# Performance work log

Hardware: AMD Instinct MI355X
Metric: run time of the kernel (lower is better)

The kernel has to match this reference:

```python
import jax, jax.numpy as jnp
import numpy as np

B = 16384
R, N_NODES, K, N_LAYERS, LATENT = 5, 68, 32, 3, 68


def setup_inputs() -> dict:
    key = jax.random.key(0)
    ks = jax.random.split(key, 6)
    z = jax.random.normal(ks[0], (B, LATENT), dtype=jnp.float32)
    adjacency = jax.random.randint(ks[1], (N_NODES, K), 0, N_NODES)
    # init_fc weights stored as [latent, n_nodes] so forward is z @ fc_w[r] + fc_b[r]
    fc_w = jax.random.normal(ks[2], (R, LATENT, N_NODES), dtype=jnp.float32) * 0.1
    fc_b = jax.random.normal(ks[3], (R, N_NODES), dtype=jnp.float32) * 0.1
    gcn_w = jax.random.normal(ks[4], (R, N_LAYERS, N_NODES, K), dtype=jnp.float32) * 0.1
    gcn_b = jax.random.normal(ks[5], (R, N_LAYERS, N_NODES), dtype=jnp.float32) * 0.1
    return {"z": z, "adjacency": adjacency, "fc_w": fc_w, "fc_b": fc_b,
            "gcn_w": gcn_w, "gcn_b": gcn_b}


def _gcn_layer(x, adjacency, w, b):
    # x: [B, N]; adjacency: [N, K] int; w: [N, K]; b: [N]
    x_nb = x[:, adjacency]                      # [B, N, K] ragged-style gather
    val = jnp.einsum('bnk,nk->bn', x_nb, w) + b  # per-node weighted neighbor sum
    return jax.nn.sigmoid(val)


def reference(z, adjacency, fc_w, fc_b, gcn_w, gcn_b):
    b = z.shape[0]
    sc_sum = jnp.zeros((b, N_NODES, N_NODES), dtype=z.dtype)
    for r in range(R):
        x = z @ fc_w[r] + fc_b[r]               # init_fc[r]
        for l in range(N_LAYERS):
            x = _gcn_layer(x, adjacency, gcn_w[r, l], gcn_b[r, l])
        # rank-1 outer product per sample: bmm(x.unsqueeze(2), x.unsqueeze(1))
        sc_sum = sc_sum + x[:, :, None] * x[:, None, :]
    sc_sum = 0.5 * (sc_sum + jnp.swapaxes(sc_sum, 1, 2))
    return sc_sum.reshape(b, -1)
```

## Files before the change

kernel.cpp:

```cpp
#include <hip/hip_runtime.h>
#include <math.h>

#define R_ 5
#define NN 68
#define KK 32
#define NL 3
#define LAT 68
#define NSL 17
#define ROWQ (NN / 4)
#define NF4 ((NN * NN) / 4)
#define BBK2 16
#define LSTR 344
#define NPREP (R_ * NL)

__global__ __launch_bounds__(256) void prep_k(
    const float* __restrict__ z, const int* __restrict__ adj,
    const float* __restrict__ gw, float* __restrict__ wd,
    float* __restrict__ zT, int B) {
  const int t = threadIdx.x;
  if (blockIdx.x < NPREP) {
    const int rl = blockIdx.x;
    __shared__ float col[NN][NN + 4];
    for (int i = t; i < NN * (NN + 4); i += 256) (&col[0][0])[i] = 0.0f;
    __syncthreads();
    if (t < NN) {
      const int n = t;
      const int* ar = adj + n * KK;
      const float* wr = gw + ((size_t)rl * NN + n) * KK;
      for (int k = 0; k < KK; ++k) col[ar[k]][n] += wr[k];
    }
    __syncthreads();
    float* wout = wd + (size_t)rl * NN * NN;
    for (int i = t; i < NN * NN; i += 256) {
      const int m = i / NN, n = i - m * NN;
      wout[i] = col[m][n];
    }
  } else {
    const int b0 = (blockIdx.x - NPREP) * 64;
    __shared__ float zls[64][LAT + 1];
    for (int idx = t; idx < 64 * ROWQ; idx += 256) {
      const int row = idx / ROWQ, q = idx - row * ROWQ;
      const float4 v =
          *reinterpret_cast<const float4*>(z + (size_t)(b0 + row) * LAT + 4 * q);
      zls[row][4 * q + 0] = v.x;
      zls[row][4 * q + 1] = v.y;
      zls[row][4 * q + 2] = v.z;
      zls[row][4 * q + 3] = v.w;
    }
    __syncthreads();
    for (int idx = t; idx < LAT * 64; idx += 256) {
      const int l = idx >> 6, bb = idx & 63;
      zT[(size_t)l * B + b0 + bb] = zls[bb][l];
    }
  }
}

__global__ __launch_bounds__(256) void chain_k(
    const float* __restrict__ zT, const float* __restrict__ fc_w,
    const float* __restrict__ fc_b, const float* __restrict__ wd,
    const float* __restrict__ gb, float* __restrict__ X, int B, int nb) {
  const int t = threadIdx.x;
  const int lane = t & 63;
  const int w = __builtin_amdgcn_readfirstlane(t >> 6);
  const int n0 = w * NSL;
  const int r = blockIdx.x / nb;
  const int b0 = (blockIdx.x - r * nb) * 64;

  __shared__ float xs[NN][64];

  for (int idx = t; idx < NN * 64; idx += 256) {
    const int m = idx >> 6;
    xs[m][idx & 63] = zT[(size_t)m * B + b0 + (idx & 63)];
  }
  __syncthreads();

  float acc[NSL];

#pragma unroll 1
  for (int stage = 0; stage < 1 + NL; ++stage) {
    const float* wb = (stage == 0) ? fc_w + (size_t)r * LAT * NN
                                   : wd + (size_t)(r * NL + stage - 1) * NN * NN;
    const float* bias = (stage == 0) ? fc_b + r * NN
                                     : gb + (size_t)(r * NL + stage - 1) * NN;
#pragma unroll
    for (int j = 0; j < NSL; ++j) acc[j] = bias[n0 + j];

#pragma unroll 1
    for (int mb = 0; mb < 4; ++mb) {
      float xmv[NSL];
#pragma unroll
      for (int k = 0; k < NSL; ++k) xmv[k] = xs[mb * NSL + k][lane];
      const float* wrb = wb + (size_t)(mb * NSL) * NN + n0;
#pragma unroll
      for (int k = 0; k < NSL; ++k) {
        const float* wr = wrb + (size_t)k * NN;
#pragma unroll
        for (int j = 0; j < NSL; ++j) acc[j] = fmaf(xmv[k], wr[j], acc[j]);
      }
    }
    if (stage > 0) {
#pragma unroll
      for (int j = 0; j < NSL; ++j)
        acc[j] = 1.0f / (1.0f + __expf(-acc[j]));
    }
    if (stage < NL) {
      __syncthreads();
#pragma unroll
      for (int j = 0; j < NSL; ++j) xs[n0 + j][lane] = acc[j];
      __syncthreads();
    }
  }

  float* Xb = X + ((size_t)r * NN + n0) * B + b0 + lane;
#pragma unroll
  for (int j = 0; j < NSL; ++j) Xb[(size_t)j * B] = acc[j];
}

__global__ __launch_bounds__(256) void outer_k(const float* __restrict__ X,
                                               float* __restrict__ out, int B) {
  const int t = threadIdx.x;
  const int b0 = blockIdx.x * BBK2;
  __shared__ float xls[BBK2 * LSTR];

  for (int idx = t; idx < R_ * NN * BBK2; idx += 256) {
    const int rn = idx >> 4, bb = idx & (BBK2 - 1);
    xls[bb * LSTR + rn] = X[(size_t)rn * B + b0 + bb];
  }
  __syncthreads();

  float4* ob = reinterpret_cast<float4*>(out) + (size_t)b0 * NF4;
  const int total = BBK2 * NF4;
  for (int fg = t; fg < total; fg += 256) {
    const int bb = fg / NF4;
    const int f = fg - bb * NF4;
    const int i = f / ROWQ;
    const int q = f - i * ROWQ;
    const float* xb = &xls[bb * LSTR];
    float4 a = make_float4(0.f, 0.f, 0.f, 0.f);
#pragma unroll
    for (int r = 0; r < R_; ++r) {
      const float xi = xb[r * NN + i];
      const float4 xj = *reinterpret_cast<const float4*>(xb + r * NN + 4 * q);
      a.x = fmaf(xi, xj.x, a.x);
      a.y = fmaf(xi, xj.y, a.y);
      a.z = fmaf(xi, xj.z, a.z);
      a.w = fmaf(xi, xj.w, a.w);
    }
    ob[fg] = a;
  }
}

extern "C" void kernel_launch(void* const* d_in, const int* in_sizes, int n_in,
                              void* d_out, int out_size, void* d_ws, size_t ws_size,
                              hipStream_t stream) {
  const float* z    = (const float*)d_in[0];
  const int*   adj  = (const int*)  d_in[1];
  const float* fc_w = (const float*)d_in[2];
  const float* fc_b = (const float*)d_in[3];
  const float* gw   = (const float*)d_in[4];
  const float* gb   = (const float*)d_in[5];
  float* out = (float*)d_out;

  const int B = in_sizes[0] / LAT;
  float* wd = (float*)d_ws;
  float* zT = wd + R_ * NL * NN * NN;
  float* X  = zT + (size_t)LAT * B;

  const int nb = B / 64;

  prep_k<<<NPREP + B / 64, 256, 0, stream>>>(z, adj, gw, wd, zT, B);
  chain_k<<<R_ * nb, 256, 0, stream>>>(zT, fc_w, fc_b, wd, gb, X, B, nb);
  outer_k<<<B / BBK2, 256, 0, stream>>>(X, out, B);
}
```

Measured before the change: 126.6 us.

## Restructure outer-product kernel to compute 4-row tiles with register-held columns

The outer_k kernel now assigns each wave 4 samples, with each lane holding its column slice of x in registers across all 17 row groups. Each row group is computed as a 4-row tile and staged in a per-wave LDS buffer, then written to global memory as contiguous float4 stores. This cuts the per-element index divisions and repeated LDS loads of the original flat loop. In exchange it adds divergent work for the 16-column tail (done only by c==0 lanes) and extra LDS round trips for the staged output.

```diff
diff --git a/kernel.cpp b/kernel.cpp
--- a/kernel.cpp
+++ b/kernel.cpp
@@ -121,6 +121,7 @@
   const int t = threadIdx.x;
   const int b0 = blockIdx.x * BBK2;
   __shared__ float xls[BBK2 * LSTR];
+  __shared__ float obuf[4][4 * 272];
 
   for (int idx = t; idx < R_ * NN * BBK2; idx += 256) {
     const int rn = idx >> 4, bb = idx & (BBK2 - 1);
@@ -128,25 +129,65 @@
   }
   __syncthreads();
 
-  float4* ob = reinterpret_cast<float4*>(out) + (size_t)b0 * NF4;
-  const int total = BBK2 * NF4;
-  for (int fg = t; fg < total; fg += 256) {
-    const int bb = fg / NF4;
-    const int f = fg - bb * NF4;
-    const int i = f / ROWQ;
-    const int q = f - i * ROWQ;
-    const float* xb = &xls[bb * LSTR];
-    float4 a = make_float4(0.f, 0.f, 0.f, 0.f);
-#pragma unroll
-    for (int r = 0; r < R_; ++r) {
-      const float xi = xb[r * NN + i];
-      const float4 xj = *reinterpret_cast<const float4*>(xb + r * NN + 4 * q);
-      a.x = fmaf(xi, xj.x, a.x);
-      a.y = fmaf(xi, xj.y, a.y);
-      a.z = fmaf(xi, xj.z, a.z);
-      a.w = fmaf(xi, xj.w, a.w);
-    }
-    ob[fg] = a;
+  const int lane = t & 63;
+  const int wv = t >> 6;
+  const int bsub = lane >> 4;
+  const int bb = wv * 4 + bsub;
+  const int c = lane & 15;
+  const float* xb = &xls[bb * LSTR];
+
+  float4 xj[R_], xj16[R_];
+#pragma unroll
+  for (int r = 0; r < R_; ++r)
+    xj[r] = *reinterpret_cast<const float4*>(xb + r * NN + 4 * c);
+#pragma unroll
+  for (int r = 0; r < R_; ++r)
+    xj16[r] = *reinterpret_cast<const float4*>(xb + r * NN + 64);
+
+  float* ow = &obuf[wv][0];
+  const float4* ow4 = reinterpret_cast<const float4*>(ow);
+  float4* out4 = reinterpret_cast<float4*>(out);
+
+#pragma unroll 1
+  for (int g = 0; g < 17; ++g) {
+    float4 xi[R_];
+#pragma unroll
+    for (int r = 0; r < R_; ++r)
+      xi[r] = *reinterpret_cast<const float4*>(xb + r * NN + 4 * g);
+#pragma unroll
+    for (int k = 0; k < 4; ++k) {
+      float4 a = make_float4(0.f, 0.f, 0.f, 0.f);
+#pragma unroll
+      for (int r = 0; r < R_; ++r) {
+        const float s = reinterpret_cast<const float*>(&xi[r])[k];
+        a.x = fmaf(s, xj[r].x, a.x);
+        a.y = fmaf(s, xj[r].y, a.y);
+        a.z = fmaf(s, xj[r].z, a.z);
+        a.w = fmaf(s, xj[r].w, a.w);
+      }
+      *reinterpret_cast<float4*>(&ow[bsub * 272 + k * NN + 4 * c]) = a;
+      if (c == 0) {
+        float4 e = make_float4(0.f, 0.f, 0.f, 0.f);
+#pragma unroll
+        for (int r = 0; r < R_; ++r) {
+          const float s = reinterpret_cast<const float*>(&xi[r])[k];
+          e.x = fmaf(s, xj16[r].x, e.x);
+          e.y = fmaf(s, xj16[r].y, e.y);
+          e.z = fmaf(s, xj16[r].z, e.z);
+          e.w = fmaf(s, xj16[r].w, e.w);
+        }
+        *reinterpret_cast<float4*>(&ow[bsub * 272 + k * NN + 64]) = e;
+      }
+    }
+#pragma unroll
+    for (int j = 0; j < 5; ++j) {
+      const int idx = j * 64 + lane;
+      if (idx < 272) {
+        const int bs2 = idx / 68;
+        const int rem = idx - bs2 * 68;
+        out4[(size_t)(b0 + wv * 4 + bs2) * NF4 + g * 68 + rem] = ow4[idx];
+      }
+    }
   }
 }
 
```

Result: slower. 129.7 us (+2.5%).
